# Kernel optimization log

Measured on AMD Instinct MI355X. Metric: run time of the kernel, lower is better.

Reference implementation:

```python
import jax, jax.numpy as jnp
import numpy as np

B, S, H = 2, 2048, 2048
NH, KVH, HD = 16, 4, 128
R = 16
LORA_SCALE = 32.0 / 16.0  # lora_alpha / lora_r
ATTN_SCALE = HD ** -0.5
NEG = -1e9


def setup_inputs() -> dict:
    key = jax.random.key(0)
    ks = jax.random.split(key, 16)
    q_dim, kv_dim = NH * HD, KVH * HD
    # RoPE tables
    inv_freq = 1.0 / (10000.0 ** (jnp.arange(0, HD, 2, dtype=jnp.float32) / HD))
    ang = jnp.arange(S, dtype=jnp.float32)[:, None] * inv_freq[None, :]  # [S, HD/2]
    emb = jnp.concatenate([ang, ang], axis=-1)  # [S, HD]
    cos = jnp.broadcast_to(jnp.cos(emb)[None], (B, S, HD))
    sin = jnp.broadcast_to(jnp.sin(emb)[None], (B, S, HD))
    # additive causal mask [B,1,S,S]
    causal = jnp.triu(jnp.full((S, S), NEG, dtype=jnp.float32), k=1)
    attention_mask = jnp.broadcast_to(causal[None, None], (B, 1, S, S))
    return {
        'hidden_states': jax.random.normal(ks[0], (B, S, H), jnp.float32),
        'cos': cos,
        'sin': sin,
        'attention_mask': attention_mask,
        'q_w': jax.random.normal(ks[1], (q_dim, H), jnp.float32) * 0.02,
        'k_w': jax.random.normal(ks[2], (kv_dim, H), jnp.float32) * 0.02,
        'v_w': jax.random.normal(ks[3], (kv_dim, H), jnp.float32) * 0.02,
        'q_b': jax.random.normal(ks[4], (q_dim,), jnp.float32) * 0.02,
        'k_b': jax.random.normal(ks[5], (kv_dim,), jnp.float32) * 0.02,
        'v_b': jax.random.normal(ks[6], (kv_dim,), jnp.float32) * 0.02,
        'q_A': jax.random.normal(ks[7], (H, R), jnp.float32) * (1.0 / np.sqrt(H)),
        'q_B': jax.random.normal(ks[8], (R, q_dim), jnp.float32) * 0.02,
        'k_A': jax.random.normal(ks[9], (H, R), jnp.float32) * (1.0 / np.sqrt(H)),
        'k_B': jax.random.normal(ks[10], (R, kv_dim), jnp.float32) * 0.02,
        'v_A': jax.random.normal(ks[11], (H, R), jnp.float32) * (1.0 / np.sqrt(H)),
        'v_B': jax.random.normal(ks[12], (R, kv_dim), jnp.float32) * 0.02,
        'o_w': jax.random.normal(ks[13], (H, H), jnp.float32) * 0.02,
    }


def _rotate_half(x):
    x1, x2 = x[..., : HD // 2], x[..., HD // 2:]
    return jnp.concatenate([-x2, x1], axis=-1)


def reference(hidden_states, cos, sin, attention_mask,
              q_w, k_w, v_w, q_b, k_b, v_b,
              q_A, q_B, k_A, k_B, v_A, v_B, o_w):
    x = hidden_states  # dropout p=0 (eval)
    # fused base + LoRA projections
    q = x @ q_w.T + q_b + LORA_SCALE * ((x @ q_A) @ q_B)  # [B,S,NH*HD]
    k = x @ k_w.T + k_b + LORA_SCALE * ((x @ k_A) @ k_B)  # [B,S,KVH*HD]
    v = x @ v_w.T + v_b + LORA_SCALE * ((x @ v_A) @ v_B)
    q = q.reshape(B, S, NH, HD).transpose(0, 2, 1, 3)   # [B,NH,S,HD]
    k = k.reshape(B, S, KVH, HD).transpose(0, 2, 1, 3)  # [B,KVH,S,HD]
    v = v.reshape(B, S, KVH, HD).transpose(0, 2, 1, 3)
    # RoPE
    c = cos[:, None]  # [B,1,S,HD]
    s = sin[:, None]
    q = q * c + _rotate_half(q) * s
    k = k * c + _rotate_half(k) * s
    # GQA: repeat kv heads
    n_rep = NH // KVH
    k = jnp.repeat(k, n_rep, axis=1)  # [B,NH,S,HD]
    v = jnp.repeat(v, n_rep, axis=1)
    scores = jnp.einsum('bhqd,bhkd->bhqk', q, k) * ATTN_SCALE
    scores = scores + attention_mask
    attn = jax.nn.softmax(scores.astype(jnp.float32), axis=-1).astype(q.dtype)
    out = jnp.einsum('bhqk,bhkd->bhqd', attn, v)
    out = out.transpose(0, 2, 1, 3).reshape(B, S, NH * HD)  # [B,S,H]
    return out @ o_w.T
```

## Files before the change

### kernel.cpp

```cpp
#include <hip/hip_runtime.h>

constexpr int cB   = 2;
constexpr int cS   = 2048;
constexpr int cH   = 2048;
constexpr int cNH  = 16;
constexpr int cKVH = 4;
constexpr int cHD  = 128;
constexpr int cQD  = 2048;
constexpr int cKVD = 512;
constexpr int cNQKV = 3072;
constexpr int cNTOK = 4096;
#define ATTN_SCALE 0.08838834764831845f
#define QSCALE 0.12751589549581288f

typedef __bf16 bf16;
typedef __attribute__((ext_vector_type(8))) __bf16 bf16x8;
typedef __attribute__((ext_vector_type(4))) __bf16 bf16x4;
typedef __attribute__((ext_vector_type(4))) float  f32x4;

__device__ __forceinline__ void async_load16(const bf16* g, bf16* l) {
    __builtin_amdgcn_global_load_lds(
        (const __attribute__((address_space(1))) void*)g,
        (__attribute__((address_space(3))) void*)l, 16, 0, 0);
}

__global__ void conv_f32_bf16(const float* __restrict__ in, bf16* __restrict__ out) {
    int i = (blockIdx.x * 256 + threadIdx.x) * 4;
    f32x4 v = *(const f32x4*)(in + i);
    bf16x4 o;
    o[0] = (bf16)v[0]; o[1] = (bf16)v[1]; o[2] = (bf16)v[2]; o[3] = (bf16)v[3];
    *(bf16x4*)(out + i) = o;
}

__global__ __launch_bounds__(256) void prep_w2(
        const float* __restrict__ qw, const float* __restrict__ kw, const float* __restrict__ vw,
        const float* __restrict__ qA, const float* __restrict__ qB,
        const float* __restrict__ kA, const float* __restrict__ kB,
        const float* __restrict__ vA, const float* __restrict__ vB,
        const float* __restrict__ qb, const float* __restrict__ kbias, const float* __restrict__ vb,
        bf16* __restrict__ Wc, float* __restrict__ biasc) {
    const int wave = threadIdx.x >> 6, lane = threadIdx.x & 63;
    const int n = blockIdx.y * 4 + wave;
    const int k0 = blockIdx.x * 512 + lane * 8;
    const float* W; const float* Am; const float* Bm; const float* bias; int nn, nd;
    if (n < cQD)             { W = qw; Am = qA; Bm = qB; bias = qb;    nn = n;               nd = cQD; }
    else if (n < cQD + cKVD) { W = kw; Am = kA; Bm = kB; bias = kbias; nn = n - cQD;         nd = cKVD; }
    else                     { W = vw; Am = vA; Bm = vB; bias = vb;    nn = n - cQD - cKVD;  nd = cKVD; }
    if (blockIdx.x == 0 && lane == 0) biasc[n] = bias[nn];
    float bm[16];
    #pragma unroll
    for (int r = 0; r < 16; ++r) bm[r] = Bm[r * nd + nn];
    const float* wrow = W + (size_t)nn * cH + k0;
    f32x4 w0 = *(const f32x4*)(wrow);
    f32x4 w1 = *(const f32x4*)(wrow + 4);
    bf16x8 o;
    #pragma unroll
    for (int j = 0; j < 8; ++j) {
        const f32x4* am = (const f32x4*)(Am + (size_t)(k0 + j) * 16);
        f32x4 a0 = am[0], a1 = am[1], a2 = am[2], a3 = am[3];
        float acc = 0.f;
        #pragma unroll
        for (int c = 0; c < 4; ++c) acc += a0[c] * bm[c] + a1[c] * bm[4 + c]
                                         + a2[c] * bm[8 + c] + a3[c] * bm[12 + c];
        const float wv = (j < 4) ? w0[j] : w1[j - 4];
        o[j] = (bf16)(wv + 2.0f * acc);
    }
    *(bf16x8*)&Wc[(size_t)n * cH + k0] = o;
}

__global__ __launch_bounds__(512, 2) void gemm_qkv2(const bf16* __restrict__ A, const bf16* __restrict__ Bw,
                                                    const float* __restrict__ bias,
                                                    const float* __restrict__ cosb, const float* __restrict__ sinb,
                                                    bf16* __restrict__ Qr, bf16* __restrict__ Kr,
                                                    bf16* __restrict__ Vt) {
    __shared__ bf16 Al[2][256 * 64];
    __shared__ bf16 Bl[2][256 * 64];
    const int tid = threadIdx.x;
    const int wave = tid >> 6, lane = tid & 63;
    const int quad = lane >> 4, l16 = lane & 15;
    const int wm = wave >> 2, wn = wave & 3;
    const int K = cH;
    constexpr int GX = cNQKV / 256;
    constexpr int NWG = GX * (cNTOK / 256);

    const int orig = blockIdx.y * GX + blockIdx.x;
    const int swz = (orig & 7) * (NWG >> 3) + (orig >> 3);
    const long bm = (long)(swz / GX) * 256;
    const long bn = (long)(swz % GX) * 256;

    f32x4 acc[8][4];
    #pragma unroll
    for (int i = 0; i < 8; ++i)
        #pragma unroll
        for (int j = 0; j < 4; ++j) acc[i][j] = f32x4{0.f, 0.f, 0.f, 0.f};

    int ago[4], slo[4];
    #pragma unroll
    for (int i2 = 0; i2 < 4; ++i2) {
        const int si = i2 * 512 + tid;
        const int row = si >> 3, c8 = si & 7;
        ago[i2] = row * K + (c8 ^ (row & 7)) * 8;
        slo[i2] = si * 8;
    }
    const size_t bmK = (size_t)bm * K, bnK = (size_t)bn * K;

    auto STAGE = [&](int tt, int bb) {
        const bf16* As_ = A  + bmK + (size_t)tt * 64;
        const bf16* Bs_ = Bw + bnK + (size_t)tt * 64;
        #pragma unroll
        for (int i2 = 0; i2 < 4; ++i2) {
            async_load16(As_ + ago[i2], &Al[bb][slo[i2]]);
            async_load16(Bs_ + ago[i2], &Bl[bb][slo[i2]]);
        }
    };

    constexpr int NT = cH / 64;
    STAGE(0, 0);
    STAGE(1, 1);
    const int sw = l16 & 7;
    const int arow = wm * 128 + l16;
    const int brow = (wn >> 1) * 128 + (wn & 1) * 32 + l16;

    for (int t = 0; t < NT; ++t) {
        const int buf = t & 1;
        if (t + 1 < NT) asm volatile("s_waitcnt vmcnt(8)" ::: "memory");
        else            asm volatile("s_waitcnt vmcnt(0)" ::: "memory");
        __builtin_amdgcn_s_barrier();
        const bf16* Ab = &Al[buf][0];
        const bf16* Bb = &Bl[buf][0];
        #pragma unroll
        for (int ih = 0; ih < 2; ++ih) {
            bf16x8 af[4][2];
            #pragma unroll
            for (int ii = 0; ii < 4; ++ii)
                #pragma unroll
                for (int ks = 0; ks < 2; ++ks)
                    af[ii][ks] = *(const bf16x8*)&Ab[(arow + (ih * 4 + ii) * 16) * 64 + (((ks * 4 + quad) ^ sw) * 8)];
            #pragma unroll
            for (int jh = 0; jh < 2; ++jh) {
                bf16x8 bfr[2][2];
                #pragma unroll
                for (int jj = 0; jj < 2; ++jj)
                    #pragma unroll
                    for (int ks = 0; ks < 2; ++ks)
                        bfr[jj][ks] = *(const bf16x8*)&Bb[(brow + jj * 16 + jh * 64) * 64 + (((ks * 4 + quad) ^ sw) * 8)];
                __builtin_amdgcn_s_setprio(1);
                #pragma unroll
                for (int ii = 0; ii < 4; ++ii)
                    #pragma unroll
                    for (int jj = 0; jj < 2; ++jj)
                        #pragma unroll
                        for (int ks = 0; ks < 2; ++ks)
                            acc[ih * 4 + ii][jh * 2 + jj] = __builtin_amdgcn_mfma_f32_16x16x32_bf16(
                                af[ii][ks], bfr[jj][ks], acc[ih * 4 + ii][jh * 2 + jj], 0, 0, 0);
                __builtin_amdgcn_s_setprio(0);
            }
        }
        asm volatile("s_waitcnt lgkmcnt(0)" ::: "memory");
        __builtin_amdgcn_s_barrier();
        if (t + 2 < NT) STAGE(t + 2, buf);
    }

    #pragma unroll
    for (int j = 0; j < 4; ++j) {
        const int nloc = (wn >> 1) * 128 + (wn & 1) * 32 + (j & 1) * 16 + (j >> 1) * 64 + l16;
        const float bv = bias[bn + nloc];
        #pragma unroll
        for (int i = 0; i < 8; ++i)
            #pragma unroll
            for (int r = 0; r < 4; ++r) acc[i][j][r] += bv;
    }

    const int head = (int)(bn >> 7) + (wn >> 1);
    if (head < cNH + cKVH) {
        const bool isQ = head < cNH;
        #pragma unroll
        for (int jlo = 0; jlo < 2; ++jlo) {
            const int d = (wn & 1) * 32 + jlo * 16 + l16;
            #pragma unroll
            for (int i = 0; i < 8; ++i)
                #pragma unroll
                for (int r = 0; r < 4; ++r) {
                    const long tok = bm + wm * 128 + i * 16 + quad * 4 + r;
                    const float cv = cosb[tok * cHD + d];
                    const float sv = sinb[tok * cHD + d];
                    const float v1 = acc[i][jlo][r], v2 = acc[i][jlo + 2][r];
                    float o1 = v1 * cv - v2 * sv;
                    float o2 = v2 * cv + v1 * sv;
                    if (isQ) { o1 *= QSCALE; o2 *= QSCALE; }
                    const int b = (int)(tok >> 11), s = (int)(tok & 2047);
                    bf16* dst = isQ
                        ? Qr + ((size_t)(b * cNH + head) * cS + s) * cHD
                        : Kr + ((size_t)(b * cKVH + (head - cNH)) * cS + s) * cHD;
                    dst[d]      = (bf16)o1;
                    dst[d + 64] = (bf16)o2;
                }
        }
    } else {
        const int kv = head - cNH - cKVH;
        const int b = (int)(bm >> 11);
        const int sbase = (int)(bm & 2047);
        #pragma unroll
        for (int j = 0; j < 4; ++j) {
            const int d = (wn & 1) * 32 + (j & 1) * 16 + (j >> 1) * 64 + l16;
            #pragma unroll
            for (int i = 0; i < 8; ++i) {
                const int s0 = sbase + wm * 128 + i * 16 + quad * 4;
                bf16x4 o4;
                #pragma unroll
                for (int r = 0; r < 4; ++r) o4[r] = (bf16)acc[i][j][r];
                *(bf16x4*)&Vt[((size_t)((b * cKVH + kv) * cHD) + d) * cS + s0] = o4;
            }
        }
    }
}

__global__ __launch_bounds__(512, 2) void gemm_oproj(const bf16* __restrict__ A, const bf16* __restrict__ Bw,
                                                     float* __restrict__ Cp) {
    __shared__ bf16 Al[2][256 * 64];
    __shared__ bf16 Bl[2][128 * 64];
    const int tid = threadIdx.x;
    const int wave = tid >> 6, lane = tid & 63;
    const int quad = lane >> 4, l16 = lane & 15;
    const int wm = wave >> 2, wn = wave & 3;
    constexpr int K = cH, N = cH;
    constexpr int GX = cH / 128;
    constexpr int NWG = GX * (cNTOK / 256);

    const int orig = blockIdx.y * GX + blockIdx.x;
    const int swz = (orig & 7) * (NWG >> 3) + (orig >> 3);
    const long bm = (long)(swz / GX) * 256;
    const long bn = (long)(swz % GX) * 128;

    f32x4 acc[8][2];
    #pragma unroll
    for (int i = 0; i < 8; ++i)
        #pragma unroll
        for (int j = 0; j < 2; ++j) acc[i][j] = f32x4{0.f, 0.f, 0.f, 0.f};

    int ago[4], aslo[4], bgo[2], bslo[2];
    #pragma unroll
    for (int i2 = 0; i2 < 4; ++i2) {
        const int si = i2 * 512 + tid;
        const int row = si >> 3, c8 = si & 7;
        ago[i2] = row * K + (c8 ^ (row & 7)) * 8;
        aslo[i2] = si * 8;
    }
    #pragma unroll
    for (int i2 = 0; i2 < 2; ++i2) {
        const int si = i2 * 512 + tid;
        const int row = si >> 3, c8 = si & 7;
        bgo[i2] = row * K + (c8 ^ (row & 7)) * 8;
        bslo[i2] = si * 8;
    }
    const size_t bmK = (size_t)bm * K, bnK = (size_t)bn * K;

    auto STAGE = [&](int tt, int bb) {
        const bf16* As_ = A  + bmK + (size_t)tt * 64;
        const bf16* Bs_ = Bw + bnK + (size_t)tt * 64;
        #pragma unroll
        for (int i2 = 0; i2 < 4; ++i2) async_load16(As_ + ago[i2], &Al[bb][aslo[i2]]);
        #pragma unroll
        for (int i2 = 0; i2 < 2; ++i2) async_load16(Bs_ + bgo[i2], &Bl[bb][bslo[i2]]);
    };

    constexpr int NT = K / 64;
    STAGE(0, 0);
    STAGE(1, 1);
    const int sw = l16 & 7;
    const int arow = wm * 128 + l16;
    const int brow = wn * 32 + l16;

    for (int t = 0; t < NT; ++t) {
        const int buf = t & 1;
        if (t + 1 < NT) asm volatile("s_waitcnt vmcnt(6)" ::: "memory");
        else            asm volatile("s_waitcnt vmcnt(0)" ::: "memory");
        __builtin_amdgcn_s_barrier();
        const bf16* Ab = &Al[buf][0];
        const bf16* Bb = &Bl[buf][0];
        bf16x8 bfr[2][2];
        #pragma unroll
        for (int jj = 0; jj < 2; ++jj)
            #pragma unroll
            for (int ks = 0; ks < 2; ++ks)
                bfr[jj][ks] = *(const bf16x8*)&Bb[(brow + jj * 16) * 64 + (((ks * 4 + quad) ^ sw) * 8)];
        #pragma unroll
        for (int ih = 0; ih < 2; ++ih) {
            bf16x8 af[4][2];
            #pragma unroll
            for (int ii = 0; ii < 4; ++ii)
                #pragma unroll
                for (int ks = 0; ks < 2; ++ks)
                    af[ii][ks] = *(const bf16x8*)&Ab[(arow + (ih * 4 + ii) * 16) * 64 + (((ks * 4 + quad) ^ sw) * 8)];
            __builtin_amdgcn_s_setprio(1);
            #pragma unroll
            for (int ii = 0; ii < 4; ++ii)
                #pragma unroll
                for (int jj = 0; jj < 2; ++jj)
                    #pragma unroll
                    for (int ks = 0; ks < 2; ++ks)
                        acc[ih * 4 + ii][jj] = __builtin_amdgcn_mfma_f32_16x16x32_bf16(
                            af[ii][ks], bfr[jj][ks], acc[ih * 4 + ii][jj], 0, 0, 0);
            __builtin_amdgcn_s_setprio(0);
        }
        asm volatile("s_waitcnt lgkmcnt(0)" ::: "memory");
        __builtin_amdgcn_s_barrier();
        if (t + 2 < NT) STAGE(t + 2, buf);
    }

    #pragma unroll
    for (int i = 0; i < 8; ++i)
        #pragma unroll
        for (int j = 0; j < 2; ++j) {
            const long m0 = bm + wm * 128 + i * 16 + quad * 4;
            const long n  = bn + wn * 32 + j * 16 + l16;
            #pragma unroll
            for (int r = 0; r < 4; ++r)
                Cp[(m0 + r) * N + n] = acc[i][j][r];
        }
}

__global__ __launch_bounds__(256, 2) void flash5(const bf16* __restrict__ Q, const bf16* __restrict__ K,
                                                 const bf16* __restrict__ Vt, bf16* __restrict__ Ob) {
    __shared__ bf16 kb[2][8192];
    __shared__ bf16 vb[2][8192];
    __shared__ bf16 pb[4096];
    const int tid = threadIdx.x;
    const int wave = tid >> 6, lane = tid & 63;
    const int quad = lane >> 4, l16 = lane & 15;
    const int pi = blockIdx.x;
    const int h = blockIdx.y, b = blockIdx.z;

    const bf16* Qh = Q  + (size_t)(b * cNH + h) * cS * cHD;
    const bf16* Kg = K  + (size_t)(b * cKVH + (h >> 2)) * cS * cHD;
    const bf16* Vg = Vt + (size_t)(b * cKVH + (h >> 2)) * cHD * cS;

    int kgo[4], vgo[4], slo[4];
    #pragma unroll
    for (int i2 = 0; i2 < 4; ++i2) {
        const int si = i2 * 256 + tid;
        const int krow = si >> 4, kcsw = si & 15;
        const int kc = (kcsw & 8) | ((kcsw & 7) ^ (krow & 7));
        kgo[i2] = krow * cHD + kc * 8;
        const int vrow = si >> 3, vcsw = si & 7;
        const int vc = vcsw ^ (vrow & 7);
        vgo[i2] = vrow * cS + vc * 8;
        slo[i2] = si * 8;
    }

    auto STAGE_KV = [&](int kt, int bb) {
        const bf16* Kt  = Kg + (size_t)kt * 64 * cHD;
        const bf16* Vtt = Vg + kt * 64;
        #pragma unroll
        for (int i2 = 0; i2 < 4; ++i2) async_load16(Kt + kgo[i2], &kb[bb][slo[i2]]);
        #pragma unroll
        for (int i2 = 0; i2 < 4; ++i2) async_load16(Vtt + vgo[i2], &vb[bb][slo[i2]]);
    };

    #pragma unroll
    for (int t2 = 0; t2 < 2; ++t2) {
        const int qt = t2 == 0 ? (31 - pi) : pi;

        const bf16* Qg = Qh + (size_t)qt * 64 * cHD;
        bf16x8 qf[4];
        #pragma unroll
        for (int ks = 0; ks < 4; ++ks)
            qf[ks] = *(const bf16x8*)(Qg + (size_t)(wave * 16 + l16) * cHD + ks * 32 + quad * 8);

        f32x4 oac[8];
        #pragma unroll
        for (int dt = 0; dt < 8; ++dt) oac[dt] = f32x4{0.f, 0.f, 0.f, 0.f};
        float m_ = -3.0e38f, l_ = 0.f;

        const int nkt = qt + 1;
        STAGE_KV(0, 0);
        for (int kt = 0; kt < nkt; ++kt) {
            const int bb = kt & 1;
            const bool more = (kt + 1 < nkt);
            if (more) STAGE_KV(kt + 1, bb ^ 1);
            if (more) asm volatile("s_waitcnt vmcnt(8)" ::: "memory");
            else      asm volatile("s_waitcnt vmcnt(0)" ::: "memory");
            __builtin_amdgcn_s_barrier();
            const bf16* kbp = &kb[bb][0];
            const bf16* vbp = &vb[bb][0];

            f32x4 st[4];
            #pragma unroll
            for (int mt = 0; mt < 4; ++mt) {
                bf16x8 kf[4];
                #pragma unroll
                for (int ks = 0; ks < 4; ++ks) {
                    const int c = ks * 4 + quad;
                    const int csw = (c & 8) | ((c & 7) ^ (l16 & 7));
                    kf[ks] = *(const bf16x8*)&kbp[(mt * 16 + l16) * 128 + csw * 8];
                }
                f32x4 a = f32x4{0.f, 0.f, 0.f, 0.f};
                __builtin_amdgcn_s_setprio(1);
                #pragma unroll
                for (int ks = 0; ks < 4; ++ks)
                    a = __builtin_amdgcn_mfma_f32_16x16x32_bf16(kf[ks], qf[ks], a, 0, 0, 0);
                __builtin_amdgcn_s_setprio(0);
                st[mt] = a;
            }

            const int qpos = qt * 64 + wave * 16 + l16;
            float tmax = -3.0e38f;
            if ((kt * 64 + 63) > (qt * 64 + wave * 16)) {
                #pragma unroll
                for (int mt = 0; mt < 4; ++mt)
                    #pragma unroll
                    for (int r = 0; r < 4; ++r) {
                        const int kpos = kt * 64 + mt * 16 + quad * 4 + r;
                        if (kpos > qpos) st[mt][r] = -3.0e38f;
                        tmax = fmaxf(tmax, st[mt][r]);
                    }
            } else {
                #pragma unroll
                for (int mt = 0; mt < 4; ++mt)
                    #pragma unroll
                    for (int r = 0; r < 4; ++r) tmax = fmaxf(tmax, st[mt][r]);
            }
            tmax = fmaxf(tmax, __shfl_xor(tmax, 16, 64));
            tmax = fmaxf(tmax, __shfl_xor(tmax, 32, 64));
            const float mnew = fmaxf(m_, tmax);
            if (__any(tmax > m_)) {
                const float alpha = __builtin_amdgcn_exp2f(m_ - mnew);
                l_ *= alpha;
                #pragma unroll
                for (int dt = 0; dt < 8; ++dt)
                    #pragma unroll
                    for (int r = 0; r < 4; ++r) oac[dt][r] *= alpha;
            }
            m_ = mnew;
            float rs = 0.f;
            #pragma unroll
            for (int mt = 0; mt < 4; ++mt)
                #pragma unroll
                for (int r = 0; r < 4; ++r) {
                    const float p = __builtin_amdgcn_exp2f(st[mt][r] - mnew);
                    st[mt][r] = p;
                    rs += p;
                }
            rs += __shfl_xor(rs, 16, 64);
            rs += __shfl_xor(rs, 32, 64);
            l_ += rs;

            #pragma unroll
            for (int mt = 0; mt < 4; ++mt) {
                bf16x4 p4;
                #pragma unroll
                for (int r = 0; r < 4; ++r) p4[r] = (bf16)st[mt][r];
                const int csw = (mt * 2 + (quad >> 1)) ^ (l16 & 7);
                *(bf16x4*)&pb[wave * 1024 + l16 * 64 + csw * 8 + (quad & 1) * 4] = p4;
            }

            bf16x8 pf[2];
            #pragma unroll
            for (int ks = 0; ks < 2; ++ks) {
                const int c = ks * 4 + quad;
                const int csw = c ^ (l16 & 7);
                pf[ks] = *(const bf16x8*)&pb[wave * 1024 + l16 * 64 + csw * 8];
            }
            #pragma unroll
            for (int dt = 0; dt < 8; ++dt) {
                bf16x8 vf[2];
                #pragma unroll
                for (int ks = 0; ks < 2; ++ks) {
                    const int c = ks * 4 + quad;
                    const int csw = c ^ (l16 & 7);
                    vf[ks] = *(const bf16x8*)&vbp[(dt * 16 + l16) * 64 + csw * 8];
                }
                __builtin_amdgcn_s_setprio(1);
                #pragma unroll
                for (int ks = 0; ks < 2; ++ks)
                    oac[dt] = __builtin_amdgcn_mfma_f32_16x16x32_bf16(vf[ks], pf[ks], oac[dt], 0, 0, 0);
                __builtin_amdgcn_s_setprio(0);
            }
            __builtin_amdgcn_s_barrier();
        }

        const float inv = 1.0f / l_;
        const int token = qt * 64 + wave * 16 + l16;
        bf16* orow = Ob + (size_t)(b * cS + token) * (cNH * cHD) + h * cHD;
        #pragma unroll
        for (int dt = 0; dt < 8; ++dt) {
            bf16x4 o4;
            #pragma unroll
            for (int r = 0; r < 4; ++r) o4[r] = (bf16)(oac[dt][r] * inv);
            *(bf16x4*)&orow[dt * 16 + quad * 4] = o4;
        }
    }
}

extern "C" void kernel_launch(void* const* d_in, const int* in_sizes, int n_in,
                              void* d_out, int out_size, void* d_ws, size_t ws_size,
                              hipStream_t stream) {
    const float* x    = (const float*)d_in[0];
    const float* cosb = (const float*)d_in[1];
    const float* sinb = (const float*)d_in[2];
    const float* qw = (const float*)d_in[4];
    const float* kw = (const float*)d_in[5];
    const float* vw = (const float*)d_in[6];
    const float* qb = (const float*)d_in[7];
    const float* kb_ = (const float*)d_in[8];
    const float* vb = (const float*)d_in[9];
    const float* qA = (const float*)d_in[10];
    const float* qB = (const float*)d_in[11];
    const float* kA = (const float*)d_in[12];
    const float* kB = (const float*)d_in[13];
    const float* vA = (const float*)d_in[14];
    const float* vB = (const float*)d_in[15];
    const float* ow = (const float*)d_in[16];
    float* out = (float*)d_out;

    char* ws = (char*)d_ws;
    bf16* Xbf   = (bf16*)ws;  ws += (size_t)cNTOK * cH * 2;
    bf16* Wc    = (bf16*)ws;  ws += (size_t)cNQKV * cH * 2;
    float* biasc = (float*)ws; ws += (size_t)cNQKV * 4;
    bf16* Qr    = (bf16*)ws;  ws += (size_t)cB * cNH * cS * cHD * 2;
    bf16* Kr    = (bf16*)ws;  ws += (size_t)cB * cKVH * cS * cHD * 2;
    bf16* Vt    = (bf16*)ws;  ws += (size_t)cB * cKVH * cHD * cS * 2;
    bf16* OWbf  = (bf16*)ws;  ws += (size_t)cH * cH * 2;
    bf16* Aout  = (bf16*)ws;  ws += (size_t)cNTOK * cQD * 2;

    conv_f32_bf16<<<(cNTOK * cH) / 1024, 256, 0, stream>>>(x, Xbf);
    conv_f32_bf16<<<(cH * cH) / 1024, 256, 0, stream>>>(ow, OWbf);
    prep_w2<<<dim3(cH / 512, cNQKV / 4), 256, 0, stream>>>(qw, kw, vw, qA, qB, kA, kB, vA, vB,
                                                           qb, kb_, vb, Wc, biasc);

    gemm_qkv2<<<dim3(cNQKV / 256, cNTOK / 256), 512, 0, stream>>>(Xbf, Wc, biasc, cosb, sinb, Qr, Kr, Vt);

    flash5<<<dim3(16, cNH, cB), 256, 0, stream>>>(Qr, Kr, Vt, Aout);

    gemm_oproj<<<dim3(cH / 128, cNTOK / 256), 512, 0, stream>>>(Aout, OWbf, out);
}
```

Baseline: 395.3 us.

## Merge prep kernels into one launch and shrink QKV GEMM tile to 128x128

The two fp32→bf16 conversion kernels and the LoRA weight-merge kernel are folded into a single launch that dispatches on block index, saving two launches and their serialisation gaps. The QKV projection GEMM moves from 256x256 tiles with 512 threads to 128x128 tiles with 256 threads. That gives 768 workgroups instead of 192, which should fill the many CUs better. In exchange, each tile reuses operands less, so global/L2 traffic per FLOP rises. The RoPE and V-transpose epilogue is remapped to the new wave layout, where each tile now covers exactly one head.

```diff
diff --git a/kernel.cpp b/kernel.cpp
--- a/kernel.cpp
+++ b/kernel.cpp
@@ -24,29 +24,42 @@
         (__attribute__((address_space(3))) void*)l, 16, 0, 0);
 }
 
-__global__ void conv_f32_bf16(const float* __restrict__ in, bf16* __restrict__ out) {
-    int i = (blockIdx.x * 256 + threadIdx.x) * 4;
-    f32x4 v = *(const f32x4*)(in + i);
-    bf16x4 o;
-    o[0] = (bf16)v[0]; o[1] = (bf16)v[1]; o[2] = (bf16)v[2]; o[3] = (bf16)v[3];
-    *(bf16x4*)(out + i) = o;
-}
-
-__global__ __launch_bounds__(256) void prep_w2(
+__global__ __launch_bounds__(256) void prep_all(
+        const float* __restrict__ x, bf16* __restrict__ Xbf,
+        const float* __restrict__ ow, bf16* __restrict__ OWbf,
         const float* __restrict__ qw, const float* __restrict__ kw, const float* __restrict__ vw,
         const float* __restrict__ qA, const float* __restrict__ qB,
         const float* __restrict__ kA, const float* __restrict__ kB,
         const float* __restrict__ vA, const float* __restrict__ vB,
         const float* __restrict__ qb, const float* __restrict__ kbias, const float* __restrict__ vb,
         bf16* __restrict__ Wc, float* __restrict__ biasc) {
+    const int bid = blockIdx.x;
+    if (bid < 8192) {
+        const int i = (bid * 256 + threadIdx.x) * 4;
+        f32x4 v = *(const f32x4*)(x + i);
+        bf16x4 o;
+        o[0] = (bf16)v[0]; o[1] = (bf16)v[1]; o[2] = (bf16)v[2]; o[3] = (bf16)v[3];
+        *(bf16x4*)(Xbf + i) = o;
+        return;
+    }
+    if (bid < 12288) {
+        const int i = ((bid - 8192) * 256 + threadIdx.x) * 4;
+        f32x4 v = *(const f32x4*)(ow + i);
+        bf16x4 o;
+        o[0] = (bf16)v[0]; o[1] = (bf16)v[1]; o[2] = (bf16)v[2]; o[3] = (bf16)v[3];
+        *(bf16x4*)(OWbf + i) = o;
+        return;
+    }
+    const int pb = bid - 12288;
+    const int bx = pb & 3, by = pb >> 2;
     const int wave = threadIdx.x >> 6, lane = threadIdx.x & 63;
-    const int n = blockIdx.y * 4 + wave;
-    const int k0 = blockIdx.x * 512 + lane * 8;
+    const int n = by * 4 + wave;
+    const int k0 = bx * 512 + lane * 8;
     const float* W; const float* Am; const float* Bm; const float* bias; int nn, nd;
     if (n < cQD)             { W = qw; Am = qA; Bm = qB; bias = qb;    nn = n;               nd = cQD; }
     else if (n < cQD + cKVD) { W = kw; Am = kA; Bm = kB; bias = kbias; nn = n - cQD;         nd = cKVD; }
     else                     { W = vw; Am = vA; Bm = vB; bias = vb;    nn = n - cQD - cKVD;  nd = cKVD; }
-    if (blockIdx.x == 0 && lane == 0) biasc[n] = bias[nn];
+    if (bx == 0 && lane == 0) biasc[n] = bias[nn];
     float bm[16];
     #pragma unroll
     for (int r = 0; r < 16; ++r) bm[r] = Bm[r * nd + nn];
@@ -68,36 +81,36 @@
     *(bf16x8*)&Wc[(size_t)n * cH + k0] = o;
 }
 
-__global__ __launch_bounds__(512, 2) void gemm_qkv2(const bf16* __restrict__ A, const bf16* __restrict__ Bw,
+__global__ __launch_bounds__(256, 2) void gemm_qkv4(const bf16* __restrict__ A, const bf16* __restrict__ Bw,
                                                     const float* __restrict__ bias,
                                                     const float* __restrict__ cosb, const float* __restrict__ sinb,
                                                     bf16* __restrict__ Qr, bf16* __restrict__ Kr,
                                                     bf16* __restrict__ Vt) {
-    __shared__ bf16 Al[2][256 * 64];
-    __shared__ bf16 Bl[2][256 * 64];
+    __shared__ bf16 Al[2][128 * 64];
+    __shared__ bf16 Bl[2][128 * 64];
     const int tid = threadIdx.x;
     const int wave = tid >> 6, lane = tid & 63;
     const int quad = lane >> 4, l16 = lane & 15;
-    const int wm = wave >> 2, wn = wave & 3;
+    const int wr = wave >> 1, wc = wave & 1;
     const int K = cH;
-    constexpr int GX = cNQKV / 256;
-    constexpr int NWG = GX * (cNTOK / 256);
+    constexpr int GX = cNQKV / 128;
+    constexpr int NWG = GX * (cNTOK / 128);
 
     const int orig = blockIdx.y * GX + blockIdx.x;
     const int swz = (orig & 7) * (NWG >> 3) + (orig >> 3);
-    const long bm = (long)(swz / GX) * 256;
-    const long bn = (long)(swz % GX) * 256;
-
-    f32x4 acc[8][4];
-    #pragma unroll
-    for (int i = 0; i < 8; ++i)
-        #pragma unroll
-        for (int j = 0; j < 4; ++j) acc[i][j] = f32x4{0.f, 0.f, 0.f, 0.f};
+    const long bm = (long)(swz / GX) * 128;
+    const long bn = (long)(swz % GX) * 128;
+
+    f32x4 acc[4][4];
+    #pragma unroll
+    for (int i = 0; i < 4; ++i)
+        #pragma unroll
+        for (int c = 0; c < 4; ++c) acc[i][c] = f32x4{0.f, 0.f, 0.f, 0.f};
 
     int ago[4], slo[4];
     #pragma unroll
     for (int i2 = 0; i2 < 4; ++i2) {
-        const int si = i2 * 512 + tid;
+        const int si = i2 * 256 + tid;
         const int row = si >> 3, c8 = si & 7;
         ago[i2] = row * K + (c8 ^ (row & 7)) * 8;
         slo[i2] = si * 8;
@@ -118,8 +131,6 @@
     STAGE(0, 0);
     STAGE(1, 1);
     const int sw = l16 & 7;
-    const int arow = wm * 128 + l16;
-    const int brow = (wn >> 1) * 128 + (wn & 1) * 32 + l16;
 
     for (int t = 0; t < NT; ++t) {
         const int buf = t & 1;
@@ -129,32 +140,25 @@
         const bf16* Ab = &Al[buf][0];
         const bf16* Bb = &Bl[buf][0];
         #pragma unroll
-        for (int ih = 0; ih < 2; ++ih) {
-            bf16x8 af[4][2];
-            #pragma unroll
-            for (int ii = 0; ii < 4; ++ii)
-                #pragma unroll
-                for (int ks = 0; ks < 2; ++ks)
-                    af[ii][ks] = *(const bf16x8*)&Ab[(arow + (ih * 4 + ii) * 16) * 64 + (((ks * 4 + quad) ^ sw) * 8)];
-            #pragma unroll
-            for (int jh = 0; jh < 2; ++jh) {
-                bf16x8 bfr[2][2];
-                #pragma unroll
-                for (int jj = 0; jj < 2; ++jj)
-                    #pragma unroll
-                    for (int ks = 0; ks < 2; ++ks)
-                        bfr[jj][ks] = *(const bf16x8*)&Bb[(brow + jj * 16 + jh * 64) * 64 + (((ks * 4 + quad) ^ sw) * 8)];
-                __builtin_amdgcn_s_setprio(1);
-                #pragma unroll
-                for (int ii = 0; ii < 4; ++ii)
-                    #pragma unroll
-                    for (int jj = 0; jj < 2; ++jj)
-                        #pragma unroll
-                        for (int ks = 0; ks < 2; ++ks)
-                            acc[ih * 4 + ii][jh * 2 + jj] = __builtin_amdgcn_mfma_f32_16x16x32_bf16(
-                                af[ii][ks], bfr[jj][ks], acc[ih * 4 + ii][jh * 2 + jj], 0, 0, 0);
-                __builtin_amdgcn_s_setprio(0);
-            }
+        for (int ks = 0; ks < 2; ++ks) {
+            const int g = ks * 4 + quad;
+            const int cofs = (g ^ sw) * 8;
+            bf16x8 af[4], bfr[4];
+            #pragma unroll
+            for (int i = 0; i < 4; ++i)
+                af[i] = *(const bf16x8*)&Ab[(wr * 64 + i * 16 + l16) * 64 + cofs];
+            #pragma unroll
+            for (int c = 0; c < 4; ++c) {
+                const int nrow = wc * 32 + (c & 1) * 16 + (c >> 1) * 64 + l16;
+                bfr[c] = *(const bf16x8*)&Bb[nrow * 64 + cofs];
+            }
+            __builtin_amdgcn_s_setprio(1);
+            #pragma unroll
+            for (int i = 0; i < 4; ++i)
+                #pragma unroll
+                for (int c = 0; c < 4; ++c)
+                    acc[i][c] = __builtin_amdgcn_mfma_f32_16x16x32_bf16(af[i], bfr[c], acc[i][c], 0, 0, 0);
+            __builtin_amdgcn_s_setprio(0);
         }
         asm volatile("s_waitcnt lgkmcnt(0)" ::: "memory");
         __builtin_amdgcn_s_barrier();
@@ -162,33 +166,33 @@
     }
 
     #pragma unroll
-    for (int j = 0; j < 4; ++j) {
-        const int nloc = (wn >> 1) * 128 + (wn & 1) * 32 + (j & 1) * 16 + (j >> 1) * 64 + l16;
+    for (int c = 0; c < 4; ++c) {
+        const int nloc = wc * 32 + (c & 1) * 16 + (c >> 1) * 64 + l16;
         const float bv = bias[bn + nloc];
         #pragma unroll
-        for (int i = 0; i < 8; ++i)
-            #pragma unroll
-            for (int r = 0; r < 4; ++r) acc[i][j][r] += bv;
-    }
-
-    const int head = (int)(bn >> 7) + (wn >> 1);
+        for (int i = 0; i < 4; ++i)
+            #pragma unroll
+            for (int r = 0; r < 4; ++r) acc[i][c][r] += bv;
+    }
+
+    const int head = (int)(bn >> 7);
     if (head < cNH + cKVH) {
         const bool isQ = head < cNH;
         #pragma unroll
-        for (int jlo = 0; jlo < 2; ++jlo) {
-            const int d = (wn & 1) * 32 + jlo * 16 + l16;
-            #pragma unroll
-            for (int i = 0; i < 8; ++i)
+        for (int cl = 0; cl < 2; ++cl) {
+            const int d = wc * 32 + cl * 16 + l16;
+            #pragma unroll
+            for (int i = 0; i < 4; ++i)
                 #pragma unroll
                 for (int r = 0; r < 4; ++r) {
-                    const long tok = bm + wm * 128 + i * 16 + quad * 4 + r;
-                    const float cv = cosb[tok * cHD + d];
-                    const float sv = sinb[tok * cHD + d];
-                    const float v1 = acc[i][jlo][r], v2 = acc[i][jlo + 2][r];
+                    const long t = bm + wr * 64 + i * 16 + quad * 4 + r;
+                    const float cv = cosb[t * cHD + d];
+                    const float sv = sinb[t * cHD + d];
+                    const float v1 = acc[i][cl][r], v2 = acc[i][cl + 2][r];
                     float o1 = v1 * cv - v2 * sv;
                     float o2 = v2 * cv + v1 * sv;
                     if (isQ) { o1 *= QSCALE; o2 *= QSCALE; }
-                    const int b = (int)(tok >> 11), s = (int)(tok & 2047);
+                    const int b = (int)(t >> 11), s = (int)(t & 2047);
                     bf16* dst = isQ
                         ? Qr + ((size_t)(b * cNH + head) * cS + s) * cHD
                         : Kr + ((size_t)(b * cKVH + (head - cNH)) * cS + s) * cHD;
@@ -201,14 +205,14 @@
         const int b = (int)(bm >> 11);
         const int sbase = (int)(bm & 2047);
         #pragma unroll
-        for (int j = 0; j < 4; ++j) {
-            const int d = (wn & 1) * 32 + (j & 1) * 16 + (j >> 1) * 64 + l16;
-            #pragma unroll
-            for (int i = 0; i < 8; ++i) {
-                const int s0 = sbase + wm * 128 + i * 16 + quad * 4;
+        for (int c = 0; c < 4; ++c) {
+            const int d = wc * 32 + (c & 1) * 16 + (c >> 1) * 64 + l16;
+            #pragma unroll
+            for (int i = 0; i < 4; ++i) {
+                const int s0 = sbase + wr * 64 + i * 16 + quad * 4;
                 bf16x4 o4;
                 #pragma unroll
-                for (int r = 0; r < 4; ++r) o4[r] = (bf16)acc[i][j][r];
+                for (int r = 0; r < 4; ++r) o4[r] = (bf16)acc[i][c][r];
                 *(bf16x4*)&Vt[((size_t)((b * cKVH + kv) * cHD) + d) * cS + s0] = o4;
             }
         }
@@ -523,12 +527,10 @@
     bf16* OWbf  = (bf16*)ws;  ws += (size_t)cH * cH * 2;
     bf16* Aout  = (bf16*)ws;  ws += (size_t)cNTOK * cQD * 2;
 
-    conv_f32_bf16<<<(cNTOK * cH) / 1024, 256, 0, stream>>>(x, Xbf);
-    conv_f32_bf16<<<(cH * cH) / 1024, 256, 0, stream>>>(ow, OWbf);
-    prep_w2<<<dim3(cH / 512, cNQKV / 4), 256, 0, stream>>>(qw, kw, vw, qA, qB, kA, kB, vA, vB,
-                                                           qb, kb_, vb, Wc, biasc);
-
-    gemm_qkv2<<<dim3(cNQKV / 256, cNTOK / 256), 512, 0, stream>>>(Xbf, Wc, biasc, cosb, sinb, Qr, Kr, Vt);
+    prep_all<<<15360, 256, 0, stream>>>(x, Xbf, ow, OWbf, qw, kw, vw, qA, qB, kA, kB, vA, vB,
+                                        qb, kb_, vb, Wc, biasc);
+
+    gemm_qkv4<<<dim3(cNQKV / 128, cNTOK / 128), 256, 0, stream>>>(Xbf, Wc, biasc, cosb, sinb, Qr, Kr, Vt);
 
     flash5<<<dim3(16, cNH, cB), 256, 0, stream>>>(Qr, Kr, Vt, Aout);
 
```

Result: no change. 387.7 us (-1.9%).
